# Performance work log

Hardware: AMD Instinct MI355X
Metric: run time of the kernel (lower is better)

Reference implementation:

```python
import jax, jax.numpy as jnp
import numpy as np

B, L, D_MODEL, H, M = 16, 512, 512, 8, 2
E = D_MODEL // H      # d_keys = d_values = 64
KMA = 25              # series-decomp moving-average kernel
KLAM = 7              # lambda conv kernel in TrendRefinement
PI = float(np.pi)


def _diff_matrix(n):
    # first-order difference matrix, shape (n-1, n)
    D = np.zeros((n - 1, n), dtype=np.float32)
    D[:, 1:] += np.eye(n - 1, dtype=np.float32)
    D[:, :-1] -= np.eye(n - 1, dtype=np.float32)
    return D


def setup_inputs() -> dict:
    key = jax.random.key(0)
    ks = jax.random.split(key, 16)
    w = lambda k, shape, s=0.02: s * jax.random.normal(k, shape, dtype=jnp.float32)
    # TrendRefinement buffers: U,S from SVD of (D2^T D2), D2 = D_{L-1} @ D_L (second difference)
    D2 = _diff_matrix(L - 1) @ _diff_matrix(L)
    U, S, _ = np.linalg.svd(D2.T @ D2)
    return {
        'queries': jax.random.normal(ks[0], (B, L, D_MODEL), dtype=jnp.float32),
        'keys':    jax.random.normal(ks[1], (B, L, D_MODEL), dtype=jnp.float32),
        'values':  jax.random.normal(ks[2], (B, L, D_MODEL), dtype=jnp.float32),
        'Wq': w(ks[3], (D_MODEL, H * E)), 'bq': jnp.zeros((H * E,), jnp.float32),
        'Wk': w(ks[4], (D_MODEL, H * E)), 'bk': jnp.zeros((H * E,), jnp.float32),
        'Wv': w(ks[5], (D_MODEL, H * E)), 'bv': jnp.zeros((H * E,), jnp.float32),
        'Wqo': w(ks[6], (D_MODEL, M * H)), 'bqo': jnp.zeros((M * H,), jnp.float32),
        'Wko': w(ks[7], (D_MODEL, M * H)), 'bko': jnp.zeros((M * H,), jnp.float32),
        'Wqt': w(ks[8], (D_MODEL, M * H)), 'bqt': jnp.zeros((M * H,), jnp.float32),
        'Wkt': w(ks[9], (D_MODEL, M * H)), 'bkt': jnp.zeros((M * H,), jnp.float32),
        'Wo': w(ks[10], (H * E, D_MODEL)), 'bo': jnp.zeros((D_MODEL,), jnp.float32),
        'Wlam': w(ks[11], (1, E, KLAM), 0.1), 'blam': jnp.zeros((1,), jnp.float32),
        'U': jnp.asarray(U, dtype=jnp.float32),
        'S': jnp.asarray(S, dtype=jnp.float32),
    }


def _mov_avg(x):
    # x: (B, L, H, E); replicate-pad then window mean of size KMA, stride 1
    pad = (KMA - 1) // 2
    xp = jnp.concatenate([jnp.repeat(x[:, :1], pad, axis=1), x,
                          jnp.repeat(x[:, -1:], pad, axis=1)], axis=1)
    c = jnp.cumsum(xp, axis=1)
    c = jnp.concatenate([jnp.zeros_like(c[:, :1]), c], axis=1)
    return (c[:, KMA:] - c[:, :-KMA]) / jnp.float32(KMA)


def _forward(queries, keys, values, Wq, bq, Wk, bk, Wv, bv, Wqo, bqo, Wko, bko,
             Wqt, bqt, Wkt, bkt, Wo, bo, Wlam, blam, U, S):
    # phase (omega/theta) projections: kernel-1 Conv1d == pointwise linear
    q_om = jax.nn.relu(queries @ Wqo + bqo).reshape(B, L, H, M)
    k_om = jax.nn.relu(keys @ Wko + bko).reshape(B, L, H, M)
    q_th = jnp.tanh(queries @ Wqt + bqt).reshape(B, L, H, M) * PI
    k_th = jnp.tanh(keys @ Wkt + bkt).reshape(B, L, H, M) * PI

    q = (queries @ Wq + bq).reshape(B, L, H, E)
    k = (keys @ Wk + bk).reshape(B, L, H, E)
    v = (values @ Wv + bv).reshape(B, L, H, E)

    # series decomposition: keep residual, keep value trend
    q = q - _mov_avg(q)
    k = k - _mov_avg(k)
    v_trend = _mov_avg(v)
    v = v - v_trend

    # inner attention: periodic-rotation-modulated softmax attention
    t = jnp.arange(L, dtype=jnp.float32)[None, :, None, None]

    def rot(x, om, th):
        phase = om * t + th                                     # (B,L,H,M)
        c, s = jnp.cos(phase), jnp.sin(phase)
        xr = jnp.concatenate([x[..., None, :] * c[..., None],
                              x[..., None, :] * s[..., None]], axis=-1)  # (B,L,H,M,2E)
        return xr.reshape(B, L, H, 2 * M * E)

    qr = rot(q, q_om, q_th)
    kr = rot(k, k_om, k_th)
    scores = jnp.einsum('blhd,bshd->bhls', qr, kr) / jnp.sqrt(jnp.float32(E))
    attn = jax.nn.softmax(scores, axis=-1)
    out = jnp.einsum('bhls,bshd->blhd', attn, v)

    # trend refinement: per-(b,h) filter g = U diag(1/(1+lambda*S)) U^T
    pad = (KLAM - 1) // 2
    vt = v_trend.transpose(0, 2, 3, 1).reshape(B * H, E, L)
    vtp = jnp.pad(vt, ((0, 0), (0, 0), (pad, pad)), mode='edge')
    lam = jax.lax.conv_general_dilated(vtp, Wlam, (1,), 'VALID',
                                       dimension_numbers=('NCH', 'OIH', 'NCH'))
    lam = lam + blam[None, :, None]
    lambdas = 1.0 + jax.nn.elu(lam).reshape(B, H, L)            # lambdas[b,h,l]
    s_scaled = lambdas * S[None, None, :]                        # (B,H,L)
    g = jnp.einsum('il,bhl,jl->bhij', U, 1.0 / (1.0 + s_scaled), U)
    out = out + jnp.einsum('bhij,bjhd->bihd', g, v_trend)

    out = out.reshape(B, L, H * E) @ Wo + bo

    # smoothness penalties
    Dq = jnp.asarray(_diff_matrix(L))
    om_pen = (jnp.sum(jnp.einsum('ji,bihm->bjhm', Dq, q_om) ** 2)
              + jnp.sum(jnp.einsum('ji,bihm->bjhm', Dq, k_om) ** 2))
    th_pen = jnp.sum(q_th ** 2) + jnp.sum(k_th ** 2)
    return out, attn, om_pen, th_pen


def reference(queries, keys, values, Wq, bq, Wk, bk, Wv, bv, Wqo, bqo, Wko, bko,
              Wqt, bqt, Wkt, bkt, Wo, bo, Wlam, blam, U, S):
    return _forward(queries, keys, values, Wq, bq, Wk, bk, Wv, bv, Wqo, bqo,
                    Wko, bko, Wqt, bqt, Wkt, bkt, Wo, bo, Wlam, blam, U, S)
```

## Files before the change

kernel.cpp:

```cpp
#include <hip/hip_runtime.h>
#include <math.h>


#define PI_F 3.14159265358979323846f

typedef __attribute__((ext_vector_type(8))) short bf16x8;
typedef __attribute__((ext_vector_type(4))) float f32x4;

static constexpr long ATTN_OFF = 4194304;
static constexpr long OM_OFF   = 37748736;
static constexpr long TH_OFF   = 37748737;

__device__ __forceinline__ ushort f2bf(float f){
  uint u = __float_as_uint(f);
  u += 0x7fffu + ((u >> 16) & 1u);
  return (ushort)(u >> 16);
}
__device__ __forceinline__ float bf2f(ushort h){
  return __uint_as_float((uint)h << 16);
}
__device__ __forceinline__ uint4 cvt8s(const float* f){
  ushort h[8];
#pragma unroll
  for (int j = 0; j < 8; j++) h[j] = f2bf(f[j]);
  uint4 H;
  H.x = (uint)h[0] | ((uint)h[1] << 16); H.y = (uint)h[2] | ((uint)h[3] << 16);
  H.z = (uint)h[4] | ((uint)h[5] << 16); H.w = (uint)h[6] | ((uint)h[7] << 16);
  return H;
}

template<int ROWS>
__device__ __forceinline__ void stage_sb(const short* __restrict__ G, int ldk,
                                         short* dst, int t){
#pragma unroll
  for (int i = 0; i < ROWS*8/256; i++){
    int p = t + i*256;
    int row = p >> 3;
    int kb = (p & 7) ^ (row & 7);
    __builtin_amdgcn_global_load_lds(
        (const __attribute__((address_space(1))) uint*)(G + (long)row*ldk + kb*8),
        (__attribute__((address_space(3))) uint*)(dst + (long)p*8), 16, 0, 0);
  }
}

template<int ROWS>
__device__ __forceinline__ void stage_sync(const short* __restrict__ G, int ldk,
                                           short* dst, int t){
#pragma unroll
  for (int i = 0; i < ROWS*8/256; i++){
    int p = t + i*256;
    int row = p >> 3, kb = p & 7;
    uint4 v = *(const uint4*)(G + (long)row*ldk + kb*8);
    *(uint4*)&dst[row*64 + ((kb ^ (row & 7)) << 3)] = v;
  }
}

template<int BM,int BN,bool QKV,int EPI>
__global__ __launch_bounds__(256)
void mgemm(int K,
  const short* __restrict__ AB, int lda, long sAb, long sAh,
  const short* __restrict__ BB, long sBb, long sBh,
  float* __restrict__ C, int ldc, long sCb, long sCh,
  const float* __restrict__ bias, const float* __restrict__ bias1, const float* __restrict__ bias2,
  const float* __restrict__ wcolp, short* __restrict__ CB, int Hdiv)
{
  __shared__ short As[BM*64], Bs[BN*64];
  constexpr int WMT = BM/2, WNT = BN/2;
  constexpr int FM = WMT/16, FN = WNT/16;

  const int z = blockIdx.z;
  const int zb = z / Hdiv, zh = z % Hdiv;
  const short* Ab = AB;
  const short* Bb = BB;
  float* Cb = C;
  short* Cbb = CB;
  if constexpr (QKV){
    Ab += (long)zb*4194304;
    if constexpr (EPI >= 4) Cbb += (long)zb*4194304;
  } else {
    Ab += (long)zb*sAb + (long)zh*sAh;
    Bb += (long)zb*sBb + (long)zh*sBh;
    if (C) Cb += (long)zb*sCb + (long)zh*sCh;
    if constexpr (EPI >= 4) Cbb += (long)zb*sCb + (long)zh*sCh;
  }

  const int t = threadIdx.x;
  const int m0 = blockIdx.y*BM, n0 = blockIdx.x*BN;
  const int wave = t >> 6, lane = t & 63;
  const int wr = wave >> 1, wc = wave & 1;
  const int lr = lane & 15, lk = lane >> 4;

  f32x4 acc[FM][FN];
#pragma unroll
  for (int mi = 0; mi < FM; mi++)
#pragma unroll
    for (int nj = 0; nj < FN; nj++) acc[mi][nj] = (f32x4){0.f, 0.f, 0.f, 0.f};

  for (int k0 = 0; k0 < K; k0 += 64){
    stage_sb<BM>(Ab + (long)m0*lda + k0, lda, As, t);
    stage_sb<BN>(Bb + (long)n0*K + k0, K, Bs, t);
    __syncthreads();
#pragma unroll
    for (int kk = 0; kk < 2; kk++){
      bf16x8 ah[FM], bh[FN];
#pragma unroll
      for (int mi = 0; mi < FM; mi++){
        int row = wr*WMT + mi*16 + lr;
        ah[mi] = *(const bf16x8*)&As[row*64 + (((kk*4 + lk) ^ (row & 7)) << 3)];
      }
#pragma unroll
      for (int nj = 0; nj < FN; nj++){
        int col = wc*WNT + nj*16 + lr;
        bh[nj] = *(const bf16x8*)&Bs[col*64 + (((kk*4 + lk) ^ (col & 7)) << 3)];
      }
#pragma unroll
      for (int mi = 0; mi < FM; mi++)
#pragma unroll
        for (int nj = 0; nj < FN; nj++)
          acc[mi][nj] = __builtin_amdgcn_mfma_f32_16x16x32_bf16(ah[mi], bh[nj], acc[mi][nj], 0, 0, 0);
    }
    __syncthreads();
  }

  const float* wz = nullptr;
  if constexpr (EPI == 4) wz = wcolp + (long)z*512;
  const float* bp = bias;
  if constexpr (QKV) bp = (zb == 0) ? bias : ((zb == 1) ? bias1 : bias2);

#pragma unroll
  for (int mi = 0; mi < FM; mi++){
#pragma unroll
    for (int r = 0; r < 4; r++){
      int grow = m0 + wr*WMT + mi*16 + lk*4 + r;
#pragma unroll
      for (int nj = 0; nj < FN; nj++){
        int gcol = n0 + wc*WNT + nj*16 + lr;
        float v = acc[mi][nj][r];
        if constexpr (EPI == 1 || EPI == 6) v += bp[gcol];
        if constexpr (EPI == 5) v += Cb[(long)grow*ldc + gcol];
        if constexpr (EPI == 4) v *= wz[gcol];
        if constexpr (EPI >= 4) Cbb[(long)grow*ldc + gcol] = (short)f2bf(v);
        else                    Cb[(long)grow*ldc + gcol] = v;
      }
    }
  }
}

__global__ __launch_bounds__(256)
void wconv_t(const float* __restrict__ W0, const float* __restrict__ W1,
             const float* __restrict__ W2, const float* __restrict__ W3,
             short* B0, short* B1, short* B2, short* B3)
{
  const float* W; short* Bp;
  switch (blockIdx.z){
    case 0:  W = W0; Bp = B0; break;
    case 1:  W = W1; Bp = B1; break;
    case 2:  W = W2; Bp = B2; break;
    default: W = W3; Bp = B3; break;
  }
  __shared__ float s[64][65];
  const int r0 = blockIdx.y*64, c0 = blockIdx.x*64;
  const int t = threadIdx.x;
#pragma unroll
  for (int i = 0; i < 4; i++){
    int idx = t + i*256;
    int r = idx >> 4, c4 = (idx & 15)*4;
    float4 v = *(const float4*)(W + (long)(r0 + r)*512 + c0 + c4);
    s[r][c4+0] = v.x; s[r][c4+1] = v.y; s[r][c4+2] = v.z; s[r][c4+3] = v.w;
  }
  __syncthreads();
#pragma unroll
  for (int i = 0; i < 2; i++){
    int p = t + i*256;
    int n = p >> 3, kb = p & 7;
    float f[8];
#pragma unroll
    for (int j = 0; j < 8; j++) f[j] = s[kb*8 + j][n];
    *(uint4*)&Bp[(long)(c0 + n)*512 + r0 + kb*8] = cvt8s(f);
  }
}

__global__ __launch_bounds__(256)
void uconv(const float* __restrict__ U, short* __restrict__ UB, short* __restrict__ UtB)
{
  __shared__ float s[64][65];
  const int r0 = blockIdx.y*64, c0 = blockIdx.x*64;
  const int t = threadIdx.x;
#pragma unroll
  for (int i = 0; i < 4; i++){
    int idx = t + i*256;
    int r = idx >> 4, c4 = (idx & 15)*4;
    float4 v = *(const float4*)(U + (long)(r0 + r)*512 + c0 + c4);
    s[r][c4+0] = v.x; s[r][c4+1] = v.y; s[r][c4+2] = v.z; s[r][c4+3] = v.w;
  }
  __syncthreads();
#pragma unroll
  for (int i = 0; i < 2; i++){
    int p = t + i*256;
    int rr = p >> 3, kb = p & 7;
    float f[8];
#pragma unroll
    for (int j = 0; j < 8; j++) f[j] = s[rr][kb*8 + j];
    *(uint4*)&UB[(long)(r0 + rr)*512 + c0 + kb*8] = cvt8s(f);
  }
#pragma unroll
  for (int i = 0; i < 2; i++){
    int p = t + i*256;
    int n = p >> 3, kb = p & 7;
    float f[8];
#pragma unroll
    for (int j = 0; j < 8; j++) f[j] = s[kb*8 + j][n];
    *(uint4*)&UtB[(long)(c0 + n)*512 + r0 + kb*8] = cvt8s(f);
  }
}

__global__ __launch_bounds__(256)
void ttcvt(const float* __restrict__ X, short* __restrict__ TB)
{
  __shared__ float s[64][65];
  const int b = blockIdx.z, l0 = blockIdx.y*64, c0 = blockIdx.x*64;
  const int t = threadIdx.x;
#pragma unroll
  for (int i = 0; i < 4; i++){
    int idx = t + i*256;
    int r = idx >> 4, c4 = (idx & 15)*4;
    float4 v = *(const float4*)(X + ((long)b*512 + l0 + r)*512 + c0 + c4);
    s[r][c4+0] = v.x; s[r][c4+1] = v.y; s[r][c4+2] = v.z; s[r][c4+3] = v.w;
  }
  __syncthreads();
#pragma unroll
  for (int i = 0; i < 2; i++){
    int p = t + i*256;
    int n = p >> 3, kb = p & 7;
    float f[8];
#pragma unroll
    for (int j = 0; j < 8; j++) f[j] = s[kb*8 + j][n];
    *(uint4*)&TB[((long)b*512 + c0 + n)*512 + l0 + kb*8] = cvt8s(f);
  }
}

__global__ __launch_bounds__(256)
void acvt(const float* __restrict__ q, const float* __restrict__ k,
          const float* __restrict__ v, short* __restrict__ base)
{
  long g = (long)blockIdx.x*256 + threadIdx.x;
  if (g >= 1572864) return;
  long idx = g & 524287; int sel = (int)(g >> 19);
  const float* src = sel == 0 ? q : (sel == 1 ? k : v);
  short* Bp = base + (long)sel*4194304;
  float f[8];
  *(float4*)&f[0] = *(const float4*)(src + idx*8);
  *(float4*)&f[4] = *(const float4*)(src + idx*8 + 4);
  *(uint4*)&Bp[idx*8] = cvt8s(f);
}

__global__ __launch_bounds__(256)
void skinny_k(const float* __restrict__ X,
              const float* __restrict__ Wom, const float* __restrict__ bom,
              const float* __restrict__ Wth, const float* __restrict__ bth,
              float* __restrict__ om_out, float* __restrict__ th_out,
              float* __restrict__ Cph)
{
    const int t = threadIdx.x;
    const int tx = t & 31, ty = t >> 5;
    const long row = (long)blockIdx.x * 8 + ty;
    const int col = tx & 15;
    const bool isTh = tx >= 16;
    const float* __restrict__ Wm = isTh ? Wth : Wom;
    const float* __restrict__ xr = X + row * 512;
    float acc0 = 0.f, acc1 = 0.f, acc2 = 0.f, acc3 = 0.f;
    for (int k = 0; k < 512; k += 4) {
        acc0 += xr[k + 0] * Wm[(k + 0) * 16 + col];
        acc1 += xr[k + 1] * Wm[(k + 1) * 16 + col];
        acc2 += xr[k + 2] * Wm[(k + 2) * 16 + col];
        acc3 += xr[k + 3] * Wm[(k + 3) * 16 + col];
    }
    float acc = (acc0 + acc1) + (acc2 + acc3);
    __shared__ float som[8][16], sth[8][16];
    float res;
    if (isTh) {
        res = tanhf(acc + bth[col]) * PI_F;
        th_out[row * 16 + col] = res;
        sth[ty][col] = res;
    } else {
        res = fmaxf(acc + bom[col], 0.f);
        om_out[row * 16 + col] = res;
        som[ty][col] = res;
    }
    __syncthreads();
    if (t < 64){
        const int r2 = t >> 3, h = t & 7;
        const long grow = (long)blockIdx.x * 8 + r2;
        const float tt = (float)(grow & 511);
        const float o0 = som[r2][h*2], o1 = som[r2][h*2+1];
        const float t0 = sth[r2][h*2], t1 = sth[r2][h*2+1];
        float c0, s0, c1, s1;
        sincosf(o0 * tt + t0, &s0, &c0);
        sincosf(o1 * tt + t1, &s1, &c1);
        float4 rr = { c0, s0, c1, s1 };
        *(float4*)&Cph[grow * 32 + h * 4] = rr;
    }
}

__global__ __launch_bounds__(256)
void movavg_all(const short* __restrict__ qpB, const short* __restrict__ kpB,
                const short* __restrict__ vpB,
                short* __restrict__ qRB, short* __restrict__ kRB,
                float* __restrict__ TREND, short* __restrict__ VTB)
{
    const int zz = blockIdx.z;
    const int src = zz >> 4, b = zz & 15;
    const int l0 = blockIdx.y * 64, c0 = blockIdx.x * 64;
    const short* XB = src == 0 ? qpB : (src == 1 ? kpB : vpB);
    short* RB = src == 0 ? qRB : kRB;
    __shared__ float sm[88][64];
    const long base = (long)b * 512 * 512 + c0;
    const int t = threadIdx.x;
    for (int i = t; i < 88 * 64; i += 256) {
        const int r = i >> 6, c = i & 63;
        int gl = l0 + r - 12;
        gl = min(max(gl, 0), 511);
        sm[r][c] = bf2f((ushort)XB[base + (long)gl * 512 + c]);
    }
    __syncthreads();
    const int tx = t & 63, ty = t >> 6;
    const int rbase = ty * 16;
    float s = 0.f;
    #pragma unroll
    for (int d = 0; d < 25; d++) s += sm[rbase + d][tx];
    const float inv = 1.f / 25.f;
    short hb[16];
    #pragma unroll
    for (int r = 0; r < 16; r++) {
        const long l = l0 + rbase + r;
        const float ma = s * inv;
        const float x = sm[rbase + r + 12][tx];
        const float res = x - ma;
        const ushort hi = f2bf(res);
        if (src < 2) {
            RB[((long)b * 512 + l) * 512 + c0 + tx] = (short)hi;
        } else {
            TREND[((long)b * 512 + l) * 512 + c0 + tx] = ma;
            hb[r] = (short)hi;
        }
        if (r < 15) s += sm[rbase + r + 25][tx] - sm[rbase + r][tx];
    }
    if (src == 2) {
        const long vo = ((long)b * 512 + c0 + tx) * 512 + l0 + rbase;
        *(uint4*)&VTB[vo]     = ((uint4*)hb)[0];
        *(uint4*)&VTB[vo + 8] = ((uint4*)hb)[1];
    }
}

__global__ __launch_bounds__(256)
void flash_k(const short* __restrict__ qB, const short* __restrict__ kB,
             const short* __restrict__ vtB,
             const float* __restrict__ Cq, const float* __restrict__ Ck,
             float* __restrict__ attn, float* __restrict__ attn_out)
{
  const int bid = blockIdx.y*8 + blockIdx.x;
  const int swz = (bid & 7)*128 + (bid >> 3);
  const int z = swz >> 3; const int b = z >> 3, h = z & 7;
  const int l0 = (swz & 7) * 64;
  const int t = threadIdx.x, wave = t >> 6, lane = t & 63;
  const int lr = lane & 15, lk = lane >> 4;

  __shared__ short SH[8192];
  __shared__ float CkS[2048];
  short* Qs = SH;
  short* Ks = SH;
  short* PPs = SH;
  short* Vs = SH + 4096;

  const int sr0 = t >> 3,          skb0 = t & 7;
  const int sr1 = (t >> 3) + 32,   skb1 = t & 7;
  const int sidx0 = sr0*64 + ((skb0 ^ (sr0 & 7)) << 3);
  const int sidx1 = sr1*64 + ((skb1 ^ (sr1 & 7)) << 3);

  stage_sync<64>(qB + ((long)(b*512 + l0))*512 + h*64, 512, Qs, t);
#pragma unroll
  for (int i = 0; i < 2; i++){
    int s = t + i*256;
    ((float4*)CkS)[s] = *(const float4*)(Ck + (((long)b*512 + s)*8 + h)*4);
  }
  __syncthreads();
  bf16x8 aq[2];
#pragma unroll
  for (int kk = 0; kk < 2; kk++){
    int row = wave*16 + lr;
    aq[kk] = *(const bf16x8*)&Qs[row*64 + (((kk*4 + lk) ^ (row & 7)) << 3)];
  }

  const long kbase0 = ((long)(b*512 + sr0))*512 + h*64 + skb0*8;
  const long kbase1 = ((long)(b*512 + sr1))*512 + h*64 + skb1*8;
  uint4 pA0, pA1, pB0, pB1;
  pA0 = *(const uint4*)(kB + kbase0);
  pA1 = *(const uint4*)(kB + kbase1);
  __syncthreads();

  f32x4 acc[32];
#pragma unroll
  for (int a = 0; a < 32; a++) acc[a] = (f32x4){0.f,0.f,0.f,0.f};
#pragma unroll
  for (int st = 0; st < 8; st++){
    if (st & 1){
      *(uint4*)&Ks[sidx0] = pB0; *(uint4*)&Ks[sidx1] = pB1;
      if (st < 7){
        pA0 = *(const uint4*)(kB + kbase0 + (long)(st+1)*64*512);
        pA1 = *(const uint4*)(kB + kbase1 + (long)(st+1)*64*512);
      }
    } else {
      *(uint4*)&Ks[sidx0] = pA0; *(uint4*)&Ks[sidx1] = pA1;
      if (st < 7){
        pB0 = *(const uint4*)(kB + kbase0 + (long)(st+1)*64*512);
        pB1 = *(const uint4*)(kB + kbase1 + (long)(st+1)*64*512);
      }
    }
    __syncthreads();
#pragma unroll
    for (int nj = 0; nj < 4; nj++){
      int srow = nj*16 + lr;
#pragma unroll
      for (int kk = 0; kk < 2; kk++){
        bf16x8 bh = *(const bf16x8*)&Ks[srow*64 + (((kk*4 + lk) ^ (srow & 7)) << 3)];
        acc[st*4+nj] = __builtin_amdgcn_mfma_f32_16x16x32_bf16(aq[kk], bh, acc[st*4+nj], 0,0,0);
      }
    }
    if (st < 7) __syncthreads();
  }

  const long vbase0 = ((long)(z*64 + sr0))*512 + skb0*8;
  const long vbase1 = ((long)(z*64 + sr1))*512 + skb1*8;
  pA0 = *(const uint4*)(vtB + vbase0);
  pA1 = *(const uint4*)(vtB + vbase1);

  float4 cqv[4];
#pragma unroll
  for (int r = 0; r < 4; r++){
    int row = l0 + wave*16 + lk*4 + r;
    cqv[r] = *(const float4*)(Cq + (((long)b*512 + row)*8 + h)*4);
  }
#pragma unroll
  for (int a = 0; a < 32; a++){
    int col = (a >> 2)*64 + (a & 3)*16 + lr;
    float4 ckv = ((float4*)CkS)[col];
#pragma unroll
    for (int r = 0; r < 4; r++){
      float mod = 0.125f*(cqv[r].x*ckv.x + cqv[r].y*ckv.y + cqv[r].z*ckv.z + cqv[r].w*ckv.w);
      acc[a][r] *= mod;
    }
  }
  float mx[4] = {-INFINITY, -INFINITY, -INFINITY, -INFINITY};
#pragma unroll
  for (int a = 0; a < 32; a++)
#pragma unroll
    for (int r = 0; r < 4; r++) mx[r] = fmaxf(mx[r], acc[a][r]);
#pragma unroll
  for (int msk = 1; msk < 16; msk <<= 1)
#pragma unroll
    for (int r = 0; r < 4; r++) mx[r] = fmaxf(mx[r], __shfl_xor(mx[r], msk));
  float sme[4] = {0.f, 0.f, 0.f, 0.f};
#pragma unroll
  for (int a = 0; a < 32; a++)
#pragma unroll
    for (int r = 0; r < 4; r++){ float e = __expf(acc[a][r] - mx[r]); acc[a][r] = e; sme[r] += e; }
#pragma unroll
  for (int msk = 1; msk < 16; msk <<= 1)
#pragma unroll
    for (int r = 0; r < 4; r++) sme[r] += __shfl_xor(sme[r], msk);
  float inv[4];
#pragma unroll
  for (int r = 0; r < 4; r++) inv[r] = 1.f / sme[r];
#pragma unroll
  for (int a = 0; a < 32; a++)
#pragma unroll
    for (int r = 0; r < 4; r++) acc[a][r] *= inv[r];

  f32x4 oacc[4];
#pragma unroll
  for (int nj = 0; nj < 4; nj++) oacc[nj] = (f32x4){0.f,0.f,0.f,0.f};
#pragma unroll
  for (int st = 0; st < 8; st++){
    __syncthreads();
#pragma unroll
    for (int a2 = 0; a2 < 4; a2++){
      int c = a2*16 + lr;
#pragma unroll
      for (int r = 0; r < 4; r++){
        int row = wave*16 + lk*4 + r;
        PPs[row*64 + (((c >> 3) ^ (row & 7)) << 3) + (c & 7)] = (short)f2bf(acc[st*4+a2][r]);
      }
    }
    if (st & 1){
      *(uint4*)&Vs[sidx0] = pB0; *(uint4*)&Vs[sidx1] = pB1;
      if (st < 7){
        pA0 = *(const uint4*)(vtB + vbase0 + (st+1)*64);
        pA1 = *(const uint4*)(vtB + vbase1 + (st+1)*64);
      }
    } else {
      *(uint4*)&Vs[sidx0] = pA0; *(uint4*)&Vs[sidx1] = pA1;
      if (st < 7){
        pB0 = *(const uint4*)(vtB + vbase0 + (st+1)*64);
        pB1 = *(const uint4*)(vtB + vbase1 + (st+1)*64);
      }
    }
#pragma unroll
    for (int a2 = 0; a2 < 4; a2++){
      int col = st*64 + a2*16 + lr;
#pragma unroll
      for (int r = 0; r < 4; r++)
        attn[((long)z*512 + l0 + wave*16 + lk*4 + r)*512 + col] = acc[st*4+a2][r];
    }
    __syncthreads();
#pragma unroll
    for (int kk = 0; kk < 2; kk++){
      int prow = wave*16 + lr;
      int phys = (kk*4 + lk) ^ (prow & 7);
      bf16x8 ah = *(const bf16x8*)&PPs[prow*64 + phys*8];
#pragma unroll
      for (int nj = 0; nj < 4; nj++){
        int vrow = nj*16 + lr;
        bf16x8 bh = *(const bf16x8*)&Vs[vrow*64 + (((kk*4 + lk) ^ (vrow & 7)) << 3)];
        oacc[nj] = __builtin_amdgcn_mfma_f32_16x16x32_bf16(ah, bh, oacc[nj], 0,0,0);
      }
    }
  }
#pragma unroll
  for (int nj = 0; nj < 4; nj++)
#pragma unroll
    for (int r = 0; r < 4; r++){
      int grow = l0 + wave*16 + lk*4 + r;
      attn_out[((long)b*512 + grow)*512 + h*64 + nj*16 + lr] = oacc[nj][r];
    }
}

__global__ __launch_bounds__(512)
void lamw_k(const float* __restrict__ VT, const float* __restrict__ Wlam,
            const float* __restrict__ blam, const float* __restrict__ Sv,
            float* __restrict__ Wout)
{
    const int z = blockIdx.x;
    const int b = z >> 3, h = z & 7;
    __shared__ float sv[512][17];
    __shared__ float sw[448];
    const int t = threadIdx.x;
    if (t < 448) sw[t] = Wlam[t];
    const float* __restrict__ Vb = VT + ((long)b * 512) * 512 + h * 64;
    float lam = 0.f;
    for (int ec = 0; ec < 4; ec++) {
        __syncthreads();
        #pragma unroll
        for (int j4 = 0; j4 < 4; j4++) {
            float4 v = *(const float4*)(Vb + (long)t * 512 + ec * 16 + j4 * 4);
            sv[t][j4 * 4 + 0] = v.x; sv[t][j4 * 4 + 1] = v.y;
            sv[t][j4 * 4 + 2] = v.z; sv[t][j4 * 4 + 3] = v.w;
        }
        __syncthreads();
        #pragma unroll
        for (int dk = 0; dk < 7; dk++) {
            int r = t + dk - 3;
            r = min(max(r, 0), 511);
            #pragma unroll
            for (int j = 0; j < 16; j++)
                lam += sv[r][j] * sw[(ec * 16 + j) * 7 + dk];
        }
    }
    lam += blam[0];
    const float el = lam > 0.f ? lam : expm1f(lam);
    const float wv = 1.f / (1.f + (1.f + el) * Sv[t]);
    Wout[(long)z * 512 + t] = wv;
}

__global__ __launch_bounds__(256)
void pen1_k(const float* __restrict__ qom, const float* __restrict__ kom,
            const float* __restrict__ qth, const float* __restrict__ kth,
            float* __restrict__ partials)
{
    const long tid = (long)blockIdx.x * 256 + threadIdx.x;
    float om = 0.f, th = 0.f;
    for (long i = tid; i < 262144; i += 65536) {
        const float* om_arr = (i < 131072) ? qom : kom;
        const float* th_arr = (i < 131072) ? qth : kth;
        const long j = i & 131071;
        const float x = th_arr[j];
        th += x * x;
        const int l = (int)((j >> 4) & 511);
        if (l < 511) {
            const float d = om_arr[j + 16] - om_arr[j];
            om += d * d;
        }
    }
    __shared__ float som[256], sth[256];
    som[threadIdx.x] = om; sth[threadIdx.x] = th;
    __syncthreads();
    for (int o = 128; o; o >>= 1) {
        if (threadIdx.x < o) {
            som[threadIdx.x] += som[threadIdx.x + o];
            sth[threadIdx.x] += sth[threadIdx.x + o];
        }
        __syncthreads();
    }
    if (threadIdx.x == 0) {
        partials[blockIdx.x] = som[0];
        partials[256 + blockIdx.x] = sth[0];
    }
}

__global__ __launch_bounds__(256)
void pen2_k(const float* __restrict__ partials, float* __restrict__ om_out,
            float* __restrict__ th_out)
{
    __shared__ float som[256], sth[256];
    const int t = threadIdx.x;
    som[t] = partials[t]; sth[t] = partials[256 + t];
    __syncthreads();
    for (int o = 128; o; o >>= 1) {
        if (t < o) { som[t] += som[t + o]; sth[t] += sth[t + o]; }
        __syncthreads();
    }
    if (t == 0) { *om_out = som[0]; *th_out = sth[0]; }
}

extern "C" void kernel_launch(void* const* d_in, const int* in_sizes, int n_in,
                              void* d_out_v, int out_size, void* d_ws, size_t ws_size,
                              hipStream_t stream)
{
    const float* queries = (const float*)d_in[0];
    const float* keys    = (const float*)d_in[1];
    const float* values  = (const float*)d_in[2];
    const float* Wq  = (const float*)d_in[3];  const float* bq  = (const float*)d_in[4];
    const float* Wk  = (const float*)d_in[5];  const float* bk  = (const float*)d_in[6];
    const float* Wv  = (const float*)d_in[7];  const float* bv  = (const float*)d_in[8];
    const float* Wqo = (const float*)d_in[9];  const float* bqo = (const float*)d_in[10];
    const float* Wko = (const float*)d_in[11]; const float* bko = (const float*)d_in[12];
    const float* Wqt = (const float*)d_in[13]; const float* bqt = (const float*)d_in[14];
    const float* Wkt = (const float*)d_in[15]; const float* bkt = (const float*)d_in[16];
    const float* Wo  = (const float*)d_in[17]; const float* bo  = (const float*)d_in[18];
    const float* Wlam= (const float*)d_in[19]; const float* blam= (const float*)d_in[20];
    const float* U   = (const float*)d_in[21]; const float* Sv  = (const float*)d_in[22];

    float* out = (float*)d_out_v;
    float* W   = (float*)d_ws;

    short* qpB = (short*)W;
    short* kpB = (short*)(W + 4194304);
    short* vpB = (short*)(W + 8388608);
    float* attn_out = W + 4194304;
    float* v_trend  = W + 12582912;
    short* R1  = (short*)(W + 16777216);
    short* qinB = R1;
    short* kinB = R1 + 4194304;
    short* vinB = R1 + 8388608;
    short* qresB = qinB;  short* kresB = kinB;  short* vtB = vinB;
    short* ttB = qresB;   short* aoB = kresB;
    short* T1tB = (short*)W;
    short* UB  = (short*)(W + 8388608);
    short* UtB = UB + 262144;
    float* q_om = W + 29360128;
    float* k_om = q_om + 131072;
    float* q_th = k_om + 131072;
    float* k_th = q_th + 131072;
    float* Cq   = k_th + 131072;
    float* Ck   = Cq + 262144;
    float* wbuf = Ck + 262144;
    float* partials = wbuf + 65536;
    short* wsp = (short*)(W + 30475264);
    short* WqB = wsp;
    short* WkB = wsp + 262144;
    short* WvB = wsp + 524288;
    short* WoB = wsp + 786432;

    float* attn = out + ATTN_OFF;
    dim3 blk(256);

    wconv_t<<<dim3(8,8,4), blk, 0, stream>>>(Wq, Wk, Wv, Wo, WqB, WkB, WvB, WoB);
    acvt<<<dim3(6144), blk, 0, stream>>>(queries, keys, values, R1);

    mgemm<128,128,true,6><<<dim3(4,64,3), blk, 0, stream>>>(
        512, qinB, 512, 0, 0, WqB, 0, 0,
        nullptr, 512, 0, 0,
        bq, bk, bv, nullptr, qpB, 1);

    skinny_k<<<dim3(1024), blk, 0, stream>>>(queries, Wqo, bqo, Wqt, bqt, q_om, q_th, Cq);
    skinny_k<<<dim3(1024), blk, 0, stream>>>(keys,    Wko, bko, Wkt, bkt, k_om, k_th, Ck);

    movavg_all<<<dim3(8,8,48), blk, 0, stream>>>(qpB, kpB, vpB,
        qresB, kresB, v_trend, vtB);

    uconv<<<dim3(8,8), blk, 0, stream>>>(U, UB, UtB);

    flash_k<<<dim3(8,128), blk, 0, stream>>>(qresB, kresB, vtB, Cq, Ck, attn, attn_out);

    ttcvt<<<dim3(8,8,16), blk, 0, stream>>>(v_trend, ttB);

    lamw_k<<<dim3(128), dim3(512), 0, stream>>>(v_trend, Wlam, blam, Sv, wbuf);

    mgemm<64,128,false,4><<<dim3(4,1,128), blk, 0, stream>>>(
        512, ttB, 512, 262144, 32768, UtB, 0, 0,
        nullptr, 512, 262144, 32768,
        nullptr, nullptr, nullptr, wbuf, T1tB, 8);

    mgemm<128,64,false,5><<<dim3(1,4,128), blk, 0, stream>>>(
        512, UB, 512, 0, 0, T1tB, 262144, 32768,
        attn_out, 512, 262144, 64,
        nullptr, nullptr, nullptr, nullptr, aoB, 8);

    mgemm<64,128,false,1><<<dim3(4,128,1), blk, 0, stream>>>(
        512, aoB, 512, 0, 0, WoB, 0, 0,
        out, 512, 0, 0,
        bo, nullptr, nullptr, nullptr, nullptr, 1);

    pen1_k<<<dim3(256), blk, 0, stream>>>(q_om, k_om, q_th, k_th, partials);
    pen2_k<<<dim3(1), blk, 0, stream>>>(partials, out + OM_OFF, out + TH_OFF);
}
```

Before: 255.6 us.

## Fuse trend transpose-convert into movavg and merge skinny projection launches

The moving-average kernel now writes the trend directly as a transposed bf16 tensor, in place of a float32 buffer. This removes the separate ttcvt transpose kernel and the fp32 trend write/read round trip. lamw_k is changed to read the bf16 transposed trend, so the lambda convolution now runs on bf16-rounded inputs. The two skinny_k launches for queries and keys are merged into one launch that uses a 2D grid.

After: 240.1 us. 1.06x faster.

```diff
diff --git a/kernel.cpp b/kernel.cpp
--- a/kernel.cpp
+++ b/kernel.cpp
@@ -215,31 +215,6 @@
 }
 
 __global__ __launch_bounds__(256)
-void ttcvt(const float* __restrict__ X, short* __restrict__ TB)
-{
-  __shared__ float s[64][65];
-  const int b = blockIdx.z, l0 = blockIdx.y*64, c0 = blockIdx.x*64;
-  const int t = threadIdx.x;
-#pragma unroll
-  for (int i = 0; i < 4; i++){
-    int idx = t + i*256;
-    int r = idx >> 4, c4 = (idx & 15)*4;
-    float4 v = *(const float4*)(X + ((long)b*512 + l0 + r)*512 + c0 + c4);
-    s[r][c4+0] = v.x; s[r][c4+1] = v.y; s[r][c4+2] = v.z; s[r][c4+3] = v.w;
-  }
-  __syncthreads();
-#pragma unroll
-  for (int i = 0; i < 2; i++){
-    int p = t + i*256;
-    int n = p >> 3, kb = p & 7;
-    float f[8];
-#pragma unroll
-    for (int j = 0; j < 8; j++) f[j] = s[kb*8 + j][n];
-    *(uint4*)&TB[((long)b*512 + c0 + n)*512 + l0 + kb*8] = cvt8s(f);
-  }
-}
-
-__global__ __launch_bounds__(256)
 void acvt(const float* __restrict__ q, const float* __restrict__ k,
           const float* __restrict__ v, short* __restrict__ base)
 {
@@ -255,12 +230,22 @@
 }
 
 __global__ __launch_bounds__(256)
-void skinny_k(const float* __restrict__ X,
-              const float* __restrict__ Wom, const float* __restrict__ bom,
-              const float* __restrict__ Wth, const float* __restrict__ bth,
-              float* __restrict__ om_out, float* __restrict__ th_out,
-              float* __restrict__ Cph)
-{
+void skinny_k(const float* __restrict__ Xq, const float* __restrict__ Xk,
+              const float* __restrict__ Wqo, const float* __restrict__ bqo,
+              const float* __restrict__ Wqt, const float* __restrict__ bqt,
+              const float* __restrict__ Wko, const float* __restrict__ bko,
+              const float* __restrict__ Wkt, const float* __restrict__ bkt,
+              float* __restrict__ q_om, float* __restrict__ q_th, float* __restrict__ Cq,
+              float* __restrict__ k_om, float* __restrict__ k_th, float* __restrict__ Ck)
+{
+    const int sel = blockIdx.y;
+    const float* X   = sel ? Xk  : Xq;
+    const float* Wom = sel ? Wko : Wqo;  const float* bom = sel ? bko : bqo;
+    const float* Wth = sel ? Wkt : Wqt;  const float* bth = sel ? bkt : bqt;
+    float* om_out = sel ? k_om : q_om;
+    float* th_out = sel ? k_th : q_th;
+    float* Cph    = sel ? Ck   : Cq;
+
     const int t = threadIdx.x;
     const int tx = t & 31, ty = t >> 5;
     const long row = (long)blockIdx.x * 8 + ty;
@@ -306,7 +291,7 @@
 void movavg_all(const short* __restrict__ qpB, const short* __restrict__ kpB,
                 const short* __restrict__ vpB,
                 short* __restrict__ qRB, short* __restrict__ kRB,
-                float* __restrict__ TREND, short* __restrict__ VTB)
+                short* __restrict__ VTB, short* __restrict__ TTB)
 {
     const int zz = blockIdx.z;
     const int src = zz >> 4, b = zz & 15;
@@ -329,19 +314,18 @@
     #pragma unroll
     for (int d = 0; d < 25; d++) s += sm[rbase + d][tx];
     const float inv = 1.f / 25.f;
-    short hb[16];
+    short hb[16], tb[16];
     #pragma unroll
     for (int r = 0; r < 16; r++) {
         const long l = l0 + rbase + r;
         const float ma = s * inv;
         const float x = sm[rbase + r + 12][tx];
         const float res = x - ma;
-        const ushort hi = f2bf(res);
         if (src < 2) {
-            RB[((long)b * 512 + l) * 512 + c0 + tx] = (short)hi;
+            RB[((long)b * 512 + l) * 512 + c0 + tx] = (short)f2bf(res);
         } else {
-            TREND[((long)b * 512 + l) * 512 + c0 + tx] = ma;
-            hb[r] = (short)hi;
+            hb[r] = (short)f2bf(res);
+            tb[r] = (short)f2bf(ma);
         }
         if (r < 15) s += sm[rbase + r + 25][tx] - sm[rbase + r][tx];
     }
@@ -349,6 +333,8 @@
         const long vo = ((long)b * 512 + c0 + tx) * 512 + l0 + rbase;
         *(uint4*)&VTB[vo]     = ((uint4*)hb)[0];
         *(uint4*)&VTB[vo + 8] = ((uint4*)hb)[1];
+        *(uint4*)&TTB[vo]     = ((uint4*)tb)[0];
+        *(uint4*)&TTB[vo + 8] = ((uint4*)tb)[1];
     }
 }
 
@@ -535,7 +521,7 @@
 }
 
 __global__ __launch_bounds__(512)
-void lamw_k(const float* __restrict__ VT, const float* __restrict__ Wlam,
+void lamw_k(const short* __restrict__ TTB, const float* __restrict__ Wlam,
             const float* __restrict__ blam, const float* __restrict__ Sv,
             float* __restrict__ Wout)
 {
@@ -545,16 +531,13 @@
     __shared__ float sw[448];
     const int t = threadIdx.x;
     if (t < 448) sw[t] = Wlam[t];
-    const float* __restrict__ Vb = VT + ((long)b * 512) * 512 + h * 64;
+    const short* __restrict__ Tb = TTB + ((long)b * 512 + h * 64) * 512;
     float lam = 0.f;
     for (int ec = 0; ec < 4; ec++) {
         __syncthreads();
         #pragma unroll
-        for (int j4 = 0; j4 < 4; j4++) {
-            float4 v = *(const float4*)(Vb + (long)t * 512 + ec * 16 + j4 * 4);
-            sv[t][j4 * 4 + 0] = v.x; sv[t][j4 * 4 + 1] = v.y;
-            sv[t][j4 * 4 + 2] = v.z; sv[t][j4 * 4 + 3] = v.w;
-        }
+        for (int j = 0; j < 16; j++)
+            sv[t][j] = bf2f((ushort)Tb[(long)(ec * 16 + j) * 512 + t]);
         __syncthreads();
         #pragma unroll
         for (int dk = 0; dk < 7; dk++) {
@@ -646,13 +629,13 @@
     short* kpB = (short*)(W + 4194304);
     short* vpB = (short*)(W + 8388608);
     float* attn_out = W + 4194304;
-    float* v_trend  = W + 12582912;
+    short* TTB = (short*)(W + 12582912);
     short* R1  = (short*)(W + 16777216);
     short* qinB = R1;
     short* kinB = R1 + 4194304;
     short* vinB = R1 + 8388608;
     short* qresB = qinB;  short* kresB = kinB;  short* vtB = vinB;
-    short* ttB = qresB;   short* aoB = kresB;
+    short* aoB = kresB;
     short* T1tB = (short*)W;
     short* UB  = (short*)(W + 8388608);
     short* UtB = UB + 262144;
@@ -681,22 +664,21 @@
         nullptr, 512, 0, 0,
         bq, bk, bv, nullptr, qpB, 1);
 
-    skinny_k<<<dim3(1024), blk, 0, stream>>>(queries, Wqo, bqo, Wqt, bqt, q_om, q_th, Cq);
-    skinny_k<<<dim3(1024), blk, 0, stream>>>(keys,    Wko, bko, Wkt, bkt, k_om, k_th, Ck);
+    skinny_k<<<dim3(1024,2), blk, 0, stream>>>(queries, keys,
+        Wqo, bqo, Wqt, bqt, Wko, bko, Wkt, bkt,
+        q_om, q_th, Cq, k_om, k_th, Ck);
 
     movavg_all<<<dim3(8,8,48), blk, 0, stream>>>(qpB, kpB, vpB,
-        qresB, kresB, v_trend, vtB);
+        qresB, kresB, vtB, TTB);
 
     uconv<<<dim3(8,8), blk, 0, stream>>>(U, UB, UtB);
 
     flash_k<<<dim3(8,128), blk, 0, stream>>>(qresB, kresB, vtB, Cq, Ck, attn, attn_out);
 
-    ttcvt<<<dim3(8,8,16), blk, 0, stream>>>(v_trend, ttB);
-
-    lamw_k<<<dim3(128), dim3(512), 0, stream>>>(v_trend, Wlam, blam, Sv, wbuf);
+    lamw_k<<<dim3(128), dim3(512), 0, stream>>>(TTB, Wlam, blam, Sv, wbuf);
 
     mgemm<64,128,false,4><<<dim3(4,1,128), blk, 0, stream>>>(
-        512, ttB, 512, 262144, 32768, UtB, 0, 0,
+        512, TTB, 512, 262144, 32768, UtB, 0, 0,
         nullptr, 512, 262144, 32768,
         nullptr, nullptr, nullptr, wbuf, T1tB, 8);
 
```
